# Kernel optimization log

Hardware: AMD Instinct MI355X
Metric: run time of the kernel (lower is better)

The kernel has to match this reference:

```python
import jax, jax.numpy as jnp
import numpy as np

B, C, M, T = 2, 512, 16, 128
H = 8
D = C // H  # 64, divisible by 4 for 2D RoPE
G = C // 4  # GroupNorm groups = 128
S = M * T


def group_norm(x, scale, bias, groups=G, eps=1e-5):
    b, c, m, t = x.shape
    xg = x.reshape(b, groups, c // groups, m, t)
    mu = xg.mean(axis=(2, 3, 4), keepdims=True)
    var = xg.var(axis=(2, 3, 4), keepdims=True)
    xn = ((xg - mu) * jax.lax.rsqrt(var + eps)).reshape(b, c, m, t)
    return xn * scale[None, :, None, None] + bias[None, :, None, None]


def dwsep_conv(x, dw, pw):
    # depthwise 3x3 (groups=C) then pointwise 1x1
    y = jax.lax.conv_general_dilated(
        x, dw, window_strides=(1, 1), padding='SAME',
        dimension_numbers=('NCHW', 'HWIO', 'NCHW'), feature_group_count=x.shape[1])
    return jnp.einsum('bcmt,cd->bdmt', y, pw)


def rope2d(x):
    # x: [B,H,M,T,D]; first D/2 dims rotated by freq index m, last D/2 by time index t
    d = x.shape[-1]
    dh = d // 2
    q = dh // 2
    inv = 1.0 / (10000.0 ** (jnp.arange(q, dtype=jnp.float32) / q))

    def rot(v, ang):
        h = v.shape[-1] // 2
        v1, v2 = v[..., :h], v[..., h:]
        c, s = jnp.cos(ang), jnp.sin(ang)
        return jnp.concatenate([v1 * c - v2 * s, v1 * s + v2 * c], axis=-1)

    ang_f = jnp.arange(x.shape[2], dtype=jnp.float32)[:, None] * inv  # [M,q]
    ang_t = jnp.arange(x.shape[3], dtype=jnp.float32)[:, None] * inv  # [T,q]
    xf = rot(x[..., :dh], ang_f[:, None, :])  # broadcast over T
    xt = rot(x[..., dh:], ang_t)
    return jnp.concatenate([xf, xt], axis=-1)


def setup_inputs() -> dict:
    key = jax.random.key(0)
    ks = jax.random.split(key, 14)
    s = 0.02
    return {
        'x': jax.random.normal(ks[0], (B, C, M, T), jnp.float32),
        'lengths': jax.random.randint(ks[1], (B,), T // 2, T + 1),
        'gn_scale': jnp.ones((C,), jnp.float32),
        'gn_bias': jnp.zeros((C,), jnp.float32),
        'dw_q': jax.random.normal(ks[2], (3, 3, 1, C), jnp.float32) * s,
        'dw_k': jax.random.normal(ks[3], (3, 3, 1, C), jnp.float32) * s,
        'dw_v': jax.random.normal(ks[4], (3, 3, 1, C), jnp.float32) * s,
        'pw_q': jax.random.normal(ks[5], (C, C), jnp.float32) * s,
        'pw_k': jax.random.normal(ks[6], (C, C), jnp.float32) * s,
        'pw_v': jax.random.normal(ks[7], (C, C), jnp.float32) * s,
        'attn_w': jax.random.normal(ks[8], (C, C), jnp.float32) * s,
        'attn_b': jnp.zeros((C,), jnp.float32),
        'out_w': jax.random.normal(ks[9], (C, C), jnp.float32) * s,
        'out_b': jnp.zeros((C,), jnp.float32),
    }


def reference(x, lengths, gn_scale, gn_bias, dw_q, dw_k, dw_v, pw_q, pw_k, pw_v,
              attn_w, attn_b, out_w, out_b):
    residual = x
    xn = group_norm(x, gn_scale, gn_bias)

    def to_heads(y):  # [B,C,M,T] -> [B,H,M,T,D]
        return y.reshape(B, H, D, M, T).transpose(0, 1, 3, 4, 2)

    q = rope2d(to_heads(dwsep_conv(xn, dw_q, pw_q)))
    k = rope2d(to_heads(dwsep_conv(xn, dw_k, pw_k)))
    v = to_heads(dwsep_conv(xn, dw_v, pw_v))

    q = q.reshape(B, H, S, D)
    k = k.reshape(B, H, S, D)
    v = v.reshape(B, H, S, D)

    scores = jnp.einsum('bhsd,bhkd->bhsk', q, k) / np.sqrt(D).astype(np.float32)
    valid_t = jnp.arange(T)[None, :] < lengths[:, None]        # [B,T]
    valid = jnp.tile(valid_t, (1, M))                          # [B,S], token idx = m*T + t
    scores = jnp.where(valid[:, None, None, :], scores, jnp.float32(-1e9))
    attn = jax.nn.softmax(scores, axis=-1)
    o = jnp.einsum('bhsk,bhkd->bhsd', attn, v)                 # [B,H,S,D]

    o = o.transpose(0, 2, 1, 3).reshape(B, S, C)
    o = o @ attn_w + attn_b                                    # block output proj
    o = o.reshape(B, M, T, C).transpose(0, 3, 1, 2)            # [B,C,M,T]
    out = jnp.einsum('bcmt,cd->bdmt', o, out_w) + out_b[None, :, None, None]
    return residual + out
```

## Files before the change

kernel.cpp:

```cpp
#include <hip/hip_runtime.h>
#include <math.h>

#define CCH 512
#define SSQ 2048
#define MTOT 4096

typedef __bf16 bf16;
typedef __bf16 bf16x8 __attribute__((ext_vector_type(8)));
typedef __bf16 bf16x4 __attribute__((ext_vector_type(4)));
typedef float  f32x4  __attribute__((ext_vector_type(4)));

#define AS1 __attribute__((address_space(1)))
#define AS3 __attribute__((address_space(3)))
__device__ __forceinline__ void glds16(const void* g, void* l) {
    __builtin_amdgcn_global_load_lds((const AS1 void*)g, (AS3 void*)l, 16, 0, 0);
}

__global__ __launch_bounds__(256) void gnw_kernel(const float* __restrict__ x,
        float* __restrict__ mu, float* __restrict__ rstd,
        const float* __restrict__ w0, const float* __restrict__ w1,
        const float* __restrict__ w2, const float* __restrict__ w3,
        const float* __restrict__ w4, bf16* __restrict__ wT) {
    __shared__ float smem[64*65];
    int tid = threadIdx.x;
    if (blockIdx.x < 256) {
        float* s_sum = smem;
        float* s_sq  = smem + 256;
        int bg = blockIdx.x;
        long base = (long)bg * 8192;
        float sum = 0.f, sq = 0.f;
#pragma unroll
        for (int r = 0; r < 32; ++r) {
            float v = x[base + r*256 + tid];
            sum += v; sq += v*v;
        }
        s_sum[tid] = sum; s_sq[tid] = sq;
        __syncthreads();
        for (int off = 128; off > 0; off >>= 1) {
            if (tid < off) { s_sum[tid] += s_sum[tid+off]; s_sq[tid] += s_sq[tid+off]; }
            __syncthreads();
        }
        if (tid == 0) {
            float m = s_sum[0] * (1.f/8192.f);
            float v = s_sq[0]  * (1.f/8192.f) - m*m;
            mu[bg] = m;
            rstd[bg] = rsqrtf(v + 1e-5f);
        }
    } else {
        int bid = blockIdx.x - 256;
        int z = bid >> 6, r2 = bid & 63;
        int k0 = (r2 >> 3)*64, n0 = (r2 & 7)*64;
        const float* srcs[5] = {w0, w1, w2, w3, w4};
        const float* W = srcs[z];
        bf16* D = wT + (long)z * (CCH*CCH);
        float (*t)[65] = (float(*)[65])smem;
        int cI = tid & 63, r4 = tid >> 6;
#pragma unroll
        for (int p = 0; p < 16; ++p) {
            int kr = p*4 + r4;
            t[kr][cI] = W[(long)(k0+kr)*CCH + n0 + cI];
        }
        __syncthreads();
#pragma unroll
        for (int p = 0; p < 16; ++p) {
            int nr = p*4 + r4;
            D[(long)(n0+nr)*CCH + k0 + cI] = (bf16)t[cI][nr];
        }
    }
}

__global__ void tn_kernel(const float* __restrict__ x, const float* __restrict__ mu,
                          const float* __restrict__ rstd, const float* __restrict__ gsc,
                          const float* __restrict__ gbs, bf16* __restrict__ xnT) {
    __shared__ float t[64][65];
    int s0 = blockIdx.x*64, c0 = blockIdx.y*64, b = blockIdx.z;
    int tid = threadIdx.x;
    int cI = tid & 63, r4 = tid >> 6;
#pragma unroll
    for (int p = 0; p < 16; ++p) {
        int cr = p*4 + r4;
        t[cr][cI] = x[((long)(b*CCH + c0 + cr))*SSQ + s0 + cI];
    }
    __syncthreads();
#pragma unroll
    for (int p = 0; p < 16; ++p) {
        int sr = p*4 + r4;
        int c = c0 + cI;
        int g = b*128 + (c >> 2);
        float v = (t[cI][sr] - mu[g]) * rstd[g] * gsc[c] + gbs[c];
        xnT[((long)(b*SSQ + s0 + sr))*CCH + c] = (bf16)v;
    }
}

__global__ __launch_bounds__(256) void dw3_kernel(const bf16* __restrict__ xnT,
        const float* __restrict__ dwq, const float* __restrict__ dwk,
        const float* __restrict__ dwv,
        bf16* __restrict__ yq, bf16* __restrict__ yk, bf16* __restrict__ yv) {
    int tid = threadIdx.x;
    int cc = (tid & 63) * 8;
    int s  = blockIdx.x*4 + (tid >> 6);
    int sl = s & (SSQ-1);
    int b  = s >> 11;
    int m = sl >> 7, t = sl & 127;
    float aq[8] = {}, ak[8] = {}, av[8] = {};
#pragma unroll
    for (int di = 0; di < 3; ++di) {
        int m2 = m + di - 1;
        if ((unsigned)m2 >= 16u) continue;
#pragma unroll
        for (int dj = 0; dj < 3; ++dj) {
            int t2 = t + dj - 1;
            if ((unsigned)t2 >= 128u) continue;
            bf16x8 xv = *(const bf16x8*)(xnT + ((long)(b*SSQ + m2*128 + t2))*CCH + cc);
            int wi = (di*3 + dj)*CCH + cc;
#pragma unroll
            for (int i = 0; i < 8; ++i) {
                float xf = (float)xv[i];
                aq[i] += xf * dwq[wi+i];
                ak[i] += xf * dwk[wi+i];
                av[i] += xf * dwv[wi+i];
            }
        }
    }
    bf16x8 oq, ok, ov;
#pragma unroll
    for (int i = 0; i < 8; ++i) { oq[i] = (bf16)aq[i]; ok[i] = (bf16)ak[i]; ov[i] = (bf16)av[i]; }
    long o = (long)s*CCH + cc;
    *(bf16x8*)(yq + o) = oq;
    *(bf16x8*)(yk + o) = ok;
    *(bf16x8*)(yv + o) = ov;
}

__device__ __forceinline__ void gemm_core(const bf16* __restrict__ A,
        const bf16* __restrict__ Wt, int m0, int n0,
        bf16* As, bf16* Bs, f32x4 acc[2][2]) {
    int tid = threadIdx.x, lane = tid & 63, wid = tid >> 6;
    int sw = wid & 1, nw = wid >> 1;
    int col = lane & 15, quad = lane >> 4;
    const char* gA[2]; const char* gB[2];
    char* ldsA[2]; char* ldsB[2];
#pragma unroll
    for (int p = 0; p < 2; ++p) {
        int ci = wid*64 + lane + p*256;
        int row = ci >> 3;
        int c = (ci & 7) ^ (row & 7);
        gA[p] = (const char*)A  + ((long)(m0+row)*CCH + c*8)*2;
        gB[p] = (const char*)Wt + ((long)(n0+row)*CCH + c*8)*2;
        ldsA[p] = (char*)As + wid*1024 + p*4096;
        ldsB[p] = (char*)Bs + wid*1024 + p*4096;
    }
    int rowA = sw*32 + col, rowB = nw*32 + col;
    for (int k0 = 0; k0 < CCH; k0 += 64) {
        __syncthreads();
#pragma unroll
        for (int p = 0; p < 2; ++p) {
            glds16(gA[p] + k0*2, ldsA[p]);
            glds16(gB[p] + k0*2, ldsB[p]);
        }
        __syncthreads();
        bf16x8 af[2][2], bfr[2][2];
#pragma unroll
        for (int mt = 0; mt < 2; ++mt) {
            int r = rowA + mt*16;
#pragma unroll
            for (int ks = 0; ks < 2; ++ks) {
                int c = (ks*4 + quad) ^ (r & 7);
                af[mt][ks] = *(const bf16x8*)((char*)As + r*128 + c*16);
            }
        }
#pragma unroll
        for (int nt = 0; nt < 2; ++nt) {
            int r = rowB + nt*16;
#pragma unroll
            for (int ks = 0; ks < 2; ++ks) {
                int c = (ks*4 + quad) ^ (r & 7);
                bfr[nt][ks] = *(const bf16x8*)((char*)Bs + r*128 + c*16);
            }
        }
#pragma unroll
        for (int ks = 0; ks < 2; ++ks)
#pragma unroll
            for (int mt = 0; mt < 2; ++mt)
#pragma unroll
                for (int nt = 0; nt < 2; ++nt)
                    acc[mt][nt] = __builtin_amdgcn_mfma_f32_16x16x32_bf16(
                        af[mt][ks], bfr[nt][ks], acc[mt][nt], 0,0,0);
    }
}

__global__ __launch_bounds__(256) void gemm_qkv(const bf16* __restrict__ Abase,
        const bf16* __restrict__ wT, bf16* __restrict__ qout,
        bf16* __restrict__ kout, bf16* __restrict__ vout) {
    __shared__ bf16 As[64*64];
    __shared__ bf16 Bs[64*64];
    int m0 = blockIdx.x*64, n0 = blockIdx.y*64, z = blockIdx.z;
    f32x4 acc[2][2] = {};
    gemm_core(Abase + (long)z*MTOT*CCH, wT + (long)z*CCH*CCH, m0, n0, As, Bs, acc);
    int tid = threadIdx.x, lane = tid & 63, wid = tid >> 6;
    int sw = wid & 1, nw = wid >> 1;
    int col = lane & 15, quad = lane >> 4;
    int nb = n0 + nw*32, mb = m0 + sw*32;
    if (z < 2) {
        bf16* outp = z ? kout : qout;
        float invf = __expf(-(float)col * 0.5756462732485114f);
        bool tHalf = (nb & 32) != 0;
        const float sc = z ? 1.0f : 0.125f;
#pragma unroll
        for (int st = 0; st < 2; ++st)
#pragma unroll
            for (int r = 0; r < 4; ++r) {
                int row = mb + st*16 + quad*4 + r;
                int sl = row & (SSQ-1);
                float pos = tHalf ? (float)(sl & 127) : (float)(sl >> 7);
                float ang = pos * invf;
                float sn, cs;
                __sincosf(ang, &sn, &cs);
                float x1 = acc[st][0][r], x2 = acc[st][1][r];
                outp[(long)row*CCH + nb + col]      = (bf16)((x1*cs - x2*sn)*sc);
                outp[(long)row*CCH + nb + 16 + col] = (bf16)((x1*sn + x2*cs)*sc);
            }
    } else {
#pragma unroll
        for (int st = 0; st < 2; ++st)
#pragma unroll
            for (int nt = 0; nt < 2; ++nt) {
                int n = nb + nt*16 + col;
                int row0 = mb + st*16 + quad*4;
                int b = row0 >> 11, sl0 = row0 & (SSQ-1);
                bf16x4 pk;
#pragma unroll
                for (int r = 0; r < 4; ++r) pk[r] = (bf16)acc[st][nt][r];
                *(bf16x4*)(vout + ((long)(b*CCH + n))*SSQ + sl0) = pk;
            }
    }
}

template<int MODE>
__global__ __launch_bounds__(256) void gemm_bf16(const bf16* __restrict__ A,
        const bf16* __restrict__ Wt, const float* __restrict__ bias,
        const float* __restrict__ resid, void* __restrict__ outv) {
    __shared__ bf16 As[64*64];
    __shared__ bf16 Bs[64*64];
    int m0 = blockIdx.x*64, n0 = blockIdx.y*64;
    f32x4 acc[2][2] = {};
    gemm_core(A, Wt, m0, n0, As, Bs, acc);
    int tid = threadIdx.x, lane = tid & 63, wid = tid >> 6;
    int sw = wid & 1, nw = wid >> 1;
    int col = lane & 15, quad = lane >> 4;
    int nb = n0 + nw*32, mb = m0 + sw*32;
    if (MODE == 3) {
        bf16* outp = (bf16*)outv;
#pragma unroll
        for (int nt = 0; nt < 2; ++nt) {
            int n = nb + nt*16 + col;
            float bv = bias[n];
#pragma unroll
            for (int st = 0; st < 2; ++st)
#pragma unroll
                for (int r = 0; r < 4; ++r)
                    outp[(long)(mb + st*16 + quad*4 + r)*CCH + n] = (bf16)(acc[st][nt][r] + bv);
        }
    } else {
        float* outp = (float*)outv;
#pragma unroll
        for (int st = 0; st < 2; ++st)
#pragma unroll
            for (int nt = 0; nt < 2; ++nt) {
                int n = nb + nt*16 + col;
                float bv = bias[n];
                int row0 = mb + st*16 + quad*4;
                int b = row0 >> 11, sl0 = row0 & (SSQ-1);
                long off = ((long)(b*CCH + n))*SSQ + sl0;
                float4 rr = *(const float4*)(resid + off);
                float4 o4;
                o4.x = acc[st][nt][0] + bv + rr.x;
                o4.y = acc[st][nt][1] + bv + rr.y;
                o4.z = acc[st][nt][2] + bv + rr.z;
                o4.w = acc[st][nt][3] + bv + rr.w;
                *(float4*)(outp + off) = o4;
            }
    }
}

#define KIMG 8192
__global__ __launch_bounds__(256) void attn_kernel(
        const bf16* __restrict__ qb, const bf16* __restrict__ kb,
        const bf16* __restrict__ vb, const int* __restrict__ lengths,
        bf16* __restrict__ o) {
    __shared__ char KVs[2*KIMG];
    __shared__ bf16 Ps[4][16*72];
    int b = blockIdx.z, h = blockIdx.y;
    int tid = threadIdx.x, wid = tid >> 6, lane = tid & 63;
    int col = lane & 15, quad = lane >> 4;
    int q0 = blockIdx.x*64 + wid*16;
    int lenb = lengths[b];

    const char* gp[4]; long gstep[4]; int ldsoff[4];
#pragma unroll
    for (int p = 0; p < 4; ++p) {
        int idx = tid + p*256;
        int isV = idx >> 9;
        int rem = idx & 511;
        int r = rem >> 3;
        int csrc = (rem & 7) ^ (r & 7);
        if (!isV) { gp[p] = (const char*)kb + ((long)(b*SSQ + r))*1024 + h*128 + csrc*16; gstep[p] = 65536; }
        else      { gp[p] = (const char*)vb + ((long)(b*CCH + h*64 + r))*4096 + csrc*16;  gstep[p] = 128; }
        ldsoff[p] = idx*16;
    }

    f32x4 vm[2][4];
#pragma unroll
    for (int p2 = 0; p2 < 2; ++p2)
#pragma unroll
        for (int sub = 0; sub < 4; ++sub)
#pragma unroll
            for (int r = 0; r < 4; ++r)
                vm[p2][sub][r] = (p2*64 + sub*16 + quad*4 + r < lenb) ? 1.f : 0.f;

    const bf16* qp = qb + (long)(b*SSQ)*CCH + h*64;
    bf16x8 qf[2];
#pragma unroll
    for (int dc = 0; dc < 2; ++dc)
        qf[dc] = *(const bf16x8*)(qp + (long)(q0 + col)*CCH + dc*32 + quad*8);

    f32x4 of[4] = {};
    float lsum = 0.f;
    bf16* pw = Ps[wid];
    int cswz = col & 7;

    bf16x8 sreg[4];
#pragma unroll
    for (int p = 0; p < 4; ++p) sreg[p] = *(const bf16x8*)(gp[p]);

    for (int t = 0; t < 32; ++t) {
        __syncthreads();
#pragma unroll
        for (int p = 0; p < 4; ++p) *(bf16x8*)(KVs + ldsoff[p]) = sreg[p];
        __syncthreads();
        if (t < 31) {
#pragma unroll
            for (int p = 0; p < 4; ++p)
                sreg[p] = *(const bf16x8*)(gp[p] + (long)(t+1)*gstep[p]);
        }
        const bf16* K = (const bf16*)KVs;
        const bf16* V = (const bf16*)(KVs + KIMG);
        int par = t & 1;
        f32x4 acc[4] = {};
#pragma unroll
        for (int sub = 0; sub < 4; ++sub)
#pragma unroll
            for (int dc = 0; dc < 2; ++dc) {
                bf16x8 kf = *(const bf16x8*)((const char*)K + (sub*16 + col)*128 + (((dc*4+quad) ^ cswz))*16);
                acc[sub] = __builtin_amdgcn_mfma_f32_16x16x32_bf16(kf, qf[dc], acc[sub], 0,0,0);
            }
#pragma unroll
        for (int sub = 0; sub < 4; ++sub) {
            bf16x4 pk;
#pragma unroll
            for (int r = 0; r < 4; ++r) {
                float p = __expf(acc[sub][r]) * vm[par][sub][r];
                lsum += p;
                pk[r] = (bf16)p;
            }
            *(bf16x4*)(pw + col*72 + sub*16 + quad*4) = pk;
        }
#pragma unroll
        for (int ks = 0; ks < 2; ++ks) {
            bf16x8 pf = *(const bf16x8*)(pw + col*72 + ks*32 + quad*8);
#pragma unroll
            for (int dt = 0; dt < 4; ++dt) {
                bf16x8 vf = *(const bf16x8*)((const char*)V + (dt*16 + col)*128 + (((ks*4+quad) ^ cswz))*16);
                of[dt] = __builtin_amdgcn_mfma_f32_16x16x32_bf16(pf, vf, of[dt], 0,0,0);
            }
        }
    }
    lsum += __shfl_xor(lsum, 16);
    lsum += __shfl_xor(lsum, 32);
    float invl = 1.f / lsum;
    float ir[4];
#pragma unroll
    for (int r = 0; r < 4; ++r) ir[r] = __shfl(invl, quad*4 + r);
    bf16* ob = o + (long)(b*SSQ + q0)*CCH + h*64;
#pragma unroll
    for (int dt = 0; dt < 4; ++dt)
#pragma unroll
        for (int r = 0; r < 4; ++r)
            ob[(long)(quad*4 + r)*CCH + dt*16 + col] = (bf16)(of[dt][r] * ir[r]);
}

extern "C" void kernel_launch(void* const* d_in, const int* in_sizes, int n_in,
                              void* d_out, int out_size, void* d_ws, size_t ws_size,
                              hipStream_t stream) {
    const float* x        = (const float*)d_in[0];
    const int*   lengths  = (const int*)  d_in[1];
    const float* gn_scale = (const float*)d_in[2];
    const float* gn_bias  = (const float*)d_in[3];
    const float* dw_q     = (const float*)d_in[4];
    const float* dw_k     = (const float*)d_in[5];
    const float* dw_v     = (const float*)d_in[6];
    const float* pw_q     = (const float*)d_in[7];
    const float* pw_k     = (const float*)d_in[8];
    const float* pw_v     = (const float*)d_in[9];
    const float* attn_w   = (const float*)d_in[10];
    const float* attn_b   = (const float*)d_in[11];
    const float* out_w    = (const float*)d_in[12];
    const float* out_b    = (const float*)d_in[13];
    float* out = (float*)d_out;

    char* w = (char*)d_ws;
    float* mu   = (float*)w;
    float* rstd = (float*)(w + 1024);
    bf16* wT    = (bf16*)(w + 4096);
    bf16* wTa = wT + 3*CCH*CCH;
    bf16* wTo = wT + 4*CCH*CCH;
    bf16* xnT  = (bf16*)(w + 0x00300000);
    bf16* yT   = (bf16*)(w + 0x00700000);
    bf16* qbf  = (bf16*)(w + 0x01300000);
    bf16* kbf  = (bf16*)(w + 0x01700000);
    bf16* vbf  = (bf16*)(w + 0x01B00000);
    bf16* obf  = (bf16*)(w + 0x01F00000);
    bf16* tmpb = (bf16*)(w + 0x02300000);

    gnw_kernel<<<576, 256, 0, stream>>>(x, mu, rstd, pw_q, pw_k, pw_v, attn_w, out_w, wT);
    tn_kernel<<<dim3(32,8,2), 256, 0, stream>>>(x, mu, rstd, gn_scale, gn_bias, xnT);
    dw3_kernel<<<MTOT/4, 256, 0, stream>>>(xnT, dw_q, dw_k, dw_v,
                                           yT, yT + (long)MTOT*CCH, yT + (long)2*MTOT*CCH);

    gemm_qkv<<<dim3(MTOT/64, CCH/64, 3), 256, 0, stream>>>(yT, wT, qbf, kbf, vbf);

    attn_kernel<<<dim3(SSQ/64, 8, 2), 256, 0, stream>>>(qbf, kbf, vbf, lengths, obf);

    dim3 gg(MTOT/64, CCH/64);
    gemm_bf16<3><<<gg, 256, 0, stream>>>(obf, wTa, attn_b, nullptr, tmpb);
    gemm_bf16<4><<<gg, 256, 0, stream>>>(tmpb, wTo, out_b, x, out);
}
```

Baseline: 166.1 us.

## Enlarge GEMM tiles to 128 rows and double-buffer attention K/V tiles

The GEMM core is generalized to 128-row tiles, with 128x128 tiles for the QKV projection and 128x64 tiles for the output projections. This raises MFMA work per LDS load and cuts the number of blocks. The attention kernel now uses two LDS buffers for K/V, so the next tile is written while the current one is consumed, leaving one barrier per iteration instead of two. In exchange, the GEMMs have fewer blocks (fewer waves to fill the CUs) and higher register use, and attention LDS use doubles, which may lower occupancy.

```diff
diff --git a/kernel.cpp b/kernel.cpp
--- a/kernel.cpp
+++ b/kernel.cpp
@@ -131,36 +131,43 @@
     *(bf16x8*)(yv + o) = ov;
 }
 
-__device__ __forceinline__ void gemm_core(const bf16* __restrict__ A,
+template<int NFR>
+__device__ __forceinline__ void gemm_core128(const bf16* __restrict__ A,
         const bf16* __restrict__ Wt, int m0, int n0,
-        bf16* As, bf16* Bs, f32x4 acc[2][2]) {
+        bf16* As, bf16* Bs, f32x4 (&acc)[4][NFR]) {
     int tid = threadIdx.x, lane = tid & 63, wid = tid >> 6;
     int sw = wid & 1, nw = wid >> 1;
     int col = lane & 15, quad = lane >> 4;
-    const char* gA[2]; const char* gB[2];
-    char* ldsA[2]; char* ldsB[2];
-#pragma unroll
-    for (int p = 0; p < 2; ++p) {
-        int ci = wid*64 + lane + p*256;
+    const char* gA[4]; char* ldsA[4];
+#pragma unroll
+    for (int p = 0; p < 4; ++p) {
+        int ci = tid + p*256;
         int row = ci >> 3;
         int c = (ci & 7) ^ (row & 7);
-        gA[p] = (const char*)A  + ((long)(m0+row)*CCH + c*8)*2;
+        gA[p] = (const char*)A + ((long)(m0+row)*CCH + c*8)*2;
+        ldsA[p] = (char*)As + ci*16;
+    }
+    const char* gB[NFR]; char* ldsB[NFR];
+#pragma unroll
+    for (int p = 0; p < NFR; ++p) {
+        int ci = tid + p*256;
+        int row = ci >> 3;
+        int c = (ci & 7) ^ (row & 7);
         gB[p] = (const char*)Wt + ((long)(n0+row)*CCH + c*8)*2;
-        ldsA[p] = (char*)As + wid*1024 + p*4096;
-        ldsB[p] = (char*)Bs + wid*1024 + p*4096;
-    }
-    int rowA = sw*32 + col, rowB = nw*32 + col;
+        ldsB[p] = (char*)Bs + ci*16;
+    }
+    int rowA = sw*64 + col;
+    int rowB = nw*(NFR*16) + col;
     for (int k0 = 0; k0 < CCH; k0 += 64) {
         __syncthreads();
 #pragma unroll
-        for (int p = 0; p < 2; ++p) {
-            glds16(gA[p] + k0*2, ldsA[p]);
-            glds16(gB[p] + k0*2, ldsB[p]);
-        }
+        for (int p = 0; p < 4; ++p)   glds16(gA[p] + k0*2, ldsA[p]);
+#pragma unroll
+        for (int p = 0; p < NFR; ++p) glds16(gB[p] + k0*2, ldsB[p]);
         __syncthreads();
-        bf16x8 af[2][2], bfr[2][2];
-#pragma unroll
-        for (int mt = 0; mt < 2; ++mt) {
+        bf16x8 af[4][2], bfr[NFR][2];
+#pragma unroll
+        for (int mt = 0; mt < 4; ++mt) {
             int r = rowA + mt*16;
 #pragma unroll
             for (int ks = 0; ks < 2; ++ks) {
@@ -169,7 +176,7 @@
             }
         }
 #pragma unroll
-        for (int nt = 0; nt < 2; ++nt) {
+        for (int nt = 0; nt < NFR; ++nt) {
             int r = rowB + nt*16;
 #pragma unroll
             for (int ks = 0; ks < 2; ++ks) {
@@ -180,9 +187,9 @@
 #pragma unroll
         for (int ks = 0; ks < 2; ++ks)
 #pragma unroll
-            for (int mt = 0; mt < 2; ++mt)
-#pragma unroll
-                for (int nt = 0; nt < 2; ++nt)
+            for (int mt = 0; mt < 4; ++mt)
+#pragma unroll
+                for (int nt = 0; nt < NFR; ++nt)
                     acc[mt][nt] = __builtin_amdgcn_mfma_f32_16x16x32_bf16(
                         af[mt][ks], bfr[nt][ks], acc[mt][nt], 0,0,0);
     }
@@ -191,45 +198,48 @@
 __global__ __launch_bounds__(256) void gemm_qkv(const bf16* __restrict__ Abase,
         const bf16* __restrict__ wT, bf16* __restrict__ qout,
         bf16* __restrict__ kout, bf16* __restrict__ vout) {
-    __shared__ bf16 As[64*64];
-    __shared__ bf16 Bs[64*64];
-    int m0 = blockIdx.x*64, n0 = blockIdx.y*64, z = blockIdx.z;
-    f32x4 acc[2][2] = {};
-    gemm_core(Abase + (long)z*MTOT*CCH, wT + (long)z*CCH*CCH, m0, n0, As, Bs, acc);
+    __shared__ bf16 As[128*64];
+    __shared__ bf16 Bs[128*64];
+    int m0 = blockIdx.x*128, n0 = blockIdx.y*128, z = blockIdx.z;
+    f32x4 acc[4][4] = {};
+    gemm_core128<4>(Abase + (long)z*MTOT*CCH, wT + (long)z*CCH*CCH, m0, n0, As, Bs, acc);
     int tid = threadIdx.x, lane = tid & 63, wid = tid >> 6;
     int sw = wid & 1, nw = wid >> 1;
     int col = lane & 15, quad = lane >> 4;
-    int nb = n0 + nw*32, mb = m0 + sw*32;
+    int nbase = n0 + nw*64;
+    int mb = m0 + sw*64;
     if (z < 2) {
         bf16* outp = z ? kout : qout;
+        const float sc = z ? 1.0f : 0.125f;
         float invf = __expf(-(float)col * 0.5756462732485114f);
-        bool tHalf = (nb & 32) != 0;
-        const float sc = z ? 1.0f : 0.125f;
-#pragma unroll
-        for (int st = 0; st < 2; ++st)
+#pragma unroll
+        for (int mt = 0; mt < 4; ++mt)
 #pragma unroll
             for (int r = 0; r < 4; ++r) {
-                int row = mb + st*16 + quad*4 + r;
+                int row = mb + mt*16 + quad*4 + r;
                 int sl = row & (SSQ-1);
-                float pos = tHalf ? (float)(sl & 127) : (float)(sl >> 7);
-                float ang = pos * invf;
-                float sn, cs;
-                __sincosf(ang, &sn, &cs);
-                float x1 = acc[st][0][r], x2 = acc[st][1][r];
-                outp[(long)row*CCH + nb + col]      = (bf16)((x1*cs - x2*sn)*sc);
-                outp[(long)row*CCH + nb + 16 + col] = (bf16)((x1*sn + x2*cs)*sc);
+#pragma unroll
+                for (int half = 0; half < 2; ++half) {
+                    float pos = half ? (float)(sl & 127) : (float)(sl >> 7);
+                    float ang = pos * invf;
+                    float sn, cs;
+                    __sincosf(ang, &sn, &cs);
+                    float x1 = acc[mt][half*2+0][r], x2 = acc[mt][half*2+1][r];
+                    outp[(long)row*CCH + nbase + half*32 + col]      = (bf16)((x1*cs - x2*sn)*sc);
+                    outp[(long)row*CCH + nbase + half*32 + 16 + col] = (bf16)((x1*sn + x2*cs)*sc);
+                }
             }
     } else {
 #pragma unroll
-        for (int st = 0; st < 2; ++st)
-#pragma unroll
-            for (int nt = 0; nt < 2; ++nt) {
-                int n = nb + nt*16 + col;
-                int row0 = mb + st*16 + quad*4;
+        for (int mt = 0; mt < 4; ++mt)
+#pragma unroll
+            for (int nt = 0; nt < 4; ++nt) {
+                int n = nbase + nt*16 + col;
+                int row0 = mb + mt*16 + quad*4;
                 int b = row0 >> 11, sl0 = row0 & (SSQ-1);
                 bf16x4 pk;
 #pragma unroll
-                for (int r = 0; r < 4; ++r) pk[r] = (bf16)acc[st][nt][r];
+                for (int r = 0; r < 4; ++r) pk[r] = (bf16)acc[mt][nt][r];
                 *(bf16x4*)(vout + ((long)(b*CCH + n))*SSQ + sl0) = pk;
             }
     }
@@ -239,15 +249,15 @@
 __global__ __launch_bounds__(256) void gemm_bf16(const bf16* __restrict__ A,
         const bf16* __restrict__ Wt, const float* __restrict__ bias,
         const float* __restrict__ resid, void* __restrict__ outv) {
-    __shared__ bf16 As[64*64];
+    __shared__ bf16 As[128*64];
     __shared__ bf16 Bs[64*64];
-    int m0 = blockIdx.x*64, n0 = blockIdx.y*64;
-    f32x4 acc[2][2] = {};
-    gemm_core(A, Wt, m0, n0, As, Bs, acc);
+    int m0 = blockIdx.x*128, n0 = blockIdx.y*64;
+    f32x4 acc[4][2] = {};
+    gemm_core128<2>(A, Wt, m0, n0, As, Bs, acc);
     int tid = threadIdx.x, lane = tid & 63, wid = tid >> 6;
     int sw = wid & 1, nw = wid >> 1;
     int col = lane & 15, quad = lane >> 4;
-    int nb = n0 + nw*32, mb = m0 + sw*32;
+    int nb = n0 + nw*32, mb = m0 + sw*64;
     if (MODE == 3) {
         bf16* outp = (bf16*)outv;
 #pragma unroll
@@ -255,28 +265,28 @@
             int n = nb + nt*16 + col;
             float bv = bias[n];
 #pragma unroll
-            for (int st = 0; st < 2; ++st)
+            for (int mt = 0; mt < 4; ++mt)
 #pragma unroll
                 for (int r = 0; r < 4; ++r)
-                    outp[(long)(mb + st*16 + quad*4 + r)*CCH + n] = (bf16)(acc[st][nt][r] + bv);
+                    outp[(long)(mb + mt*16 + quad*4 + r)*CCH + n] = (bf16)(acc[mt][nt][r] + bv);
         }
     } else {
         float* outp = (float*)outv;
 #pragma unroll
-        for (int st = 0; st < 2; ++st)
+        for (int mt = 0; mt < 4; ++mt)
 #pragma unroll
             for (int nt = 0; nt < 2; ++nt) {
                 int n = nb + nt*16 + col;
                 float bv = bias[n];
-                int row0 = mb + st*16 + quad*4;
+                int row0 = mb + mt*16 + quad*4;
                 int b = row0 >> 11, sl0 = row0 & (SSQ-1);
                 long off = ((long)(b*CCH + n))*SSQ + sl0;
                 float4 rr = *(const float4*)(resid + off);
                 float4 o4;
-                o4.x = acc[st][nt][0] + bv + rr.x;
-                o4.y = acc[st][nt][1] + bv + rr.y;
-                o4.z = acc[st][nt][2] + bv + rr.z;
-                o4.w = acc[st][nt][3] + bv + rr.w;
+                o4.x = acc[mt][nt][0] + bv + rr.x;
+                o4.y = acc[mt][nt][1] + bv + rr.y;
+                o4.z = acc[mt][nt][2] + bv + rr.z;
+                o4.w = acc[mt][nt][3] + bv + rr.w;
                 *(float4*)(outp + off) = o4;
             }
     }
@@ -287,7 +297,7 @@
         const bf16* __restrict__ qb, const bf16* __restrict__ kb,
         const bf16* __restrict__ vb, const int* __restrict__ lengths,
         bf16* __restrict__ o) {
-    __shared__ char KVs[2*KIMG];
+    __shared__ char KVs[2][2*KIMG];
     __shared__ bf16 Ps[4][16*72];
     int b = blockIdx.z, h = blockIdx.y;
     int tid = threadIdx.x, wid = tid >> 6, lane = tid & 63;
@@ -331,19 +341,15 @@
     bf16x8 sreg[4];
 #pragma unroll
     for (int p = 0; p < 4; ++p) sreg[p] = *(const bf16x8*)(gp[p]);
+#pragma unroll
+    for (int p = 0; p < 4; ++p) *(bf16x8*)(KVs[0] + ldsoff[p]) = sreg[p];
+#pragma unroll
+    for (int p = 0; p < 4; ++p) sreg[p] = *(const bf16x8*)(gp[p] + gstep[p]);
+    __syncthreads();
 
     for (int t = 0; t < 32; ++t) {
-        __syncthreads();
-#pragma unroll
-        for (int p = 0; p < 4; ++p) *(bf16x8*)(KVs + ldsoff[p]) = sreg[p];
-        __syncthreads();
-        if (t < 31) {
-#pragma unroll
-            for (int p = 0; p < 4; ++p)
-                sreg[p] = *(const bf16x8*)(gp[p] + (long)(t+1)*gstep[p]);
-        }
-        const bf16* K = (const bf16*)KVs;
-        const bf16* V = (const bf16*)(KVs + KIMG);
+        const bf16* K = (const bf16*)(KVs[t & 1]);
+        const bf16* V = (const bf16*)(KVs[t & 1] + KIMG);
         int par = t & 1;
         f32x4 acc[4] = {};
 #pragma unroll
@@ -373,6 +379,16 @@
                 of[dt] = __builtin_amdgcn_mfma_f32_16x16x32_bf16(pf, vf, of[dt], 0,0,0);
             }
         }
+        if (t < 31) {
+            char* nbuf = KVs[(t + 1) & 1];
+#pragma unroll
+            for (int p = 0; p < 4; ++p) *(bf16x8*)(nbuf + ldsoff[p]) = sreg[p];
+            if (t < 30)
+#pragma unroll
+                for (int p = 0; p < 4; ++p)
+                    sreg[p] = *(const bf16x8*)(gp[p] + (long)(t + 2) * gstep[p]);
+        }
+        __syncthreads();
     }
     lsum += __shfl_xor(lsum, 16);
     lsum += __shfl_xor(lsum, 32);
@@ -426,11 +442,11 @@
     dw3_kernel<<<MTOT/4, 256, 0, stream>>>(xnT, dw_q, dw_k, dw_v,
                                            yT, yT + (long)MTOT*CCH, yT + (long)2*MTOT*CCH);
 
-    gemm_qkv<<<dim3(MTOT/64, CCH/64, 3), 256, 0, stream>>>(yT, wT, qbf, kbf, vbf);
+    gemm_qkv<<<dim3(MTOT/128, CCH/128, 3), 256, 0, stream>>>(yT, wT, qbf, kbf, vbf);
 
     attn_kernel<<<dim3(SSQ/64, 8, 2), 256, 0, stream>>>(qbf, kbf, vbf, lengths, obf);
 
-    dim3 gg(MTOT/64, CCH/64);
+    dim3 gg(MTOT/128, CCH/64);
     gemm_bf16<3><<<gg, 256, 0, stream>>>(obf, wTa, attn_b, nullptr, tmpb);
     gemm_bf16<4><<<gg, 256, 0, stream>>>(tmpb, wTo, out_b, x, out);
 }
```

Result: slower. 172.5 us (+3.9%).
